# Kernel optimization log

Measured on AMD Instinct MI355X. Metric: run time of the kernel, lower is better.

The kernel has to match this reference:

```python
import jax, jax.numpy as jnp
import numpy as np

IN_DIM = 128
DIM = 32
N_HEADS = 4
LN_EPS = 1e-5


def setup_inputs() -> dict:
    key = jax.random.key(0)
    ks = jax.random.split(key, 10)
    B, N = 1, 256
    z = jax.random.normal(ks[0], (B, N, N, IN_DIM), dtype=jnp.float32)
    src_mask = jax.random.randint(ks[1], (B, N), 0, 2, dtype=jnp.int32)
    s = 1.0 / np.sqrt(IN_DIM)
    # weights stored in (in, out) layout: y = x @ W + b
    return {
        "z": z,
        "src_mask": src_mask,
        "ln_g": jnp.ones((IN_DIM,), jnp.float32),
        "ln_b": jnp.zeros((IN_DIM,), jnp.float32),
        "w_qkv": jax.random.normal(ks[2], (IN_DIM, 3 * N_HEADS * DIM), jnp.float32) * s,
        "w_pair": jax.random.normal(ks[3], (IN_DIM, N_HEADS), jnp.float32) * s,
        "w_gate": jax.random.normal(ks[4], (IN_DIM, IN_DIM), jnp.float32) * s,
        "b_gate": jnp.zeros((IN_DIM,), jnp.float32),
        "w_out": jax.random.normal(ks[5], (N_HEADS * DIM, IN_DIM), jnp.float32) * s,
        "b_out": jnp.zeros((IN_DIM,), jnp.float32),
    }


def reference(z, src_mask, ln_g, ln_b, w_qkv, w_pair, w_gate, b_gate, w_out, b_out):
    B, N, _, _ = z.shape
    H, D = N_HEADS, DIM
    # src_mask: zeros -> -1 (as in the torch in-place assignment)
    m = jnp.where(src_mask == 0, -1.0, 1.0).astype(z.dtype)  # [B, N]
    attn_mask = m[:, :, None] * m[:, None, :]                # [B, N, N], -1 where exactly one is masked
    # LayerNorm over last dim
    mu = jnp.mean(z, axis=-1, keepdims=True)
    var = jnp.mean(jnp.square(z - mu), axis=-1, keepdims=True)
    zn = (z - mu) / jnp.sqrt(var + LN_EPS) * ln_g + ln_b
    # QKV projection (no bias)
    qkv = zn @ w_qkv                                         # [B, N, N, 3*H*D]
    q, k, v = jnp.split(qkv, 3, axis=-1)
    q = q.reshape(B, N, N, H, D)
    k = k.reshape(B, N, N, H, D)
    v = v.reshape(B, N, N, H, D)
    pb = zn @ w_pair                                         # [B, N, N, H] pair bias
    gate = jax.nn.sigmoid(zn @ w_gate + b_gate)              # [B, N, N, IN_DIM]
    scale = float(np.sqrt(D))
    # row-wise triangle attention: attend over j within each row r
    logits = jnp.einsum('brihd,brjhd->brijh', q, k) / scale  # [B, N(r), N(i), N(j), H]
    logits = logits + pb[:, None, :, :, :]                   # bias broadcast over r
    # faithful to torch: masked positions set to -1e-9 (not -inf)
    logits = jnp.where(attn_mask[:, None, :, :, None] == -1, jnp.asarray(-1e-9, logits.dtype), logits)
    attn = jax.nn.softmax(logits, axis=3)
    out = jnp.einsum('brijh,brjhd->brihd', attn, v)          # [B, N, N, H, D]
    out = gate * out.reshape(B, N, N, H * D)
    return out @ w_out + b_out
```

## Files before the change

### kernel.cpp

```cpp
#include <hip/hip_runtime.h>
#include <hip/hip_bf16.h>
#include <math.h>


#define NPOS 65536
#define LN_EPS 1e-5f
#define SCALE_L2E 0.25503487f
#define MASKVAL  -1.4426950e-9f

typedef __attribute__((ext_vector_type(8))) short bf16x8;
typedef __attribute__((ext_vector_type(4))) float f32x4;

__device__ __forceinline__ short f2b(float f) {
    union { float f; unsigned u; } c; c.f = f;
    unsigned r = c.u + 0x7FFFu + ((c.u >> 16) & 1u);
    return (short)(r >> 16);
}
__device__ __forceinline__ unsigned cvt_pk(float lo, float hi) {
    unsigned r;
    asm("v_cvt_pk_bf16_f32 %0, %1, %2" : "=v"(r) : "v"(lo), "v"(hi));
    return r;
}
__device__ __forceinline__ float b2f_lo(unsigned u) {
    union { unsigned u; float f; } c; c.u = u << 16; return c.f;
}
__device__ __forceinline__ float b2f_hi(unsigned u) {
    union { unsigned u; float f; } c; c.u = u & 0xFFFF0000u; return c.f;
}

__global__ void k_prep(const float* __restrict__ wq, const float* __restrict__ wg,
                       const float* __restrict__ wp, const float* __restrict__ wo,
                       const int* __restrict__ smask,
                       short* __restrict__ wT, short* __restrict__ woT,
                       unsigned* __restrict__ mjbg)
{
    const int idx = blockIdx.x * 256 + threadIdx.x;
    const int stride = gridDim.x * 256;
    for (int i = idx; i < 528 * 128; i += stride) {
        const int o = i >> 7, c = i & 127;
        float v;
        if (o < 384)      v = wq[c * 384 + o];
        else if (o < 512) v = wg[c * 128 + (o - 384)];
        else if (o < 516) v = wp[c * 4 + (o - 512)] * 1.4426950408889634f;
        else              v = 0.f;
        wT[i] = f2b(v);
    }
    for (int i = idx; i < 128 * 128; i += stride) {
        const int o = i >> 7, c = i & 127;
        woT[i] = f2b(wo[c * 128 + o]);
    }
    if (blockIdx.x == 0 && threadIdx.x < 8) {
        const int gr = threadIdx.x >> 1, hw = threadIdx.x & 1;
        unsigned wbits = 0;
        for (int b = 0; b < 32; ++b) {
            const int k = hw * 32 + b;
            const int j = (k >> 2) * 16 + gr * 4 + (k & 3);
            if (smask[j] == 0) wbits |= (1u << b);
        }
        mjbg[threadIdx.x] = wbits;
    }
}

__global__ __launch_bounds__(256, 4) void k_proj(
    const float* __restrict__ z, const float* __restrict__ ln_g,
    const float* __restrict__ ln_b, const short* __restrict__ wT,
    const float* __restrict__ b_gate, short* __restrict__ qkbT,
    short* __restrict__ Vtb, float* __restrict__ pbf, short* __restrict__ gate_c)
{
    __shared__ short sBuf[17920];
    const int t = threadIdx.x, w = t >> 6, l = t & 63;
    const int lg = l & 15, gr = l >> 4;
    const int p0 = blockIdx.x * 64;
    const f32x4 zero4 = {0.f, 0.f, 0.f, 0.f};
    short* sV = sBuf;
    short* sZn = sBuf + 9216;
    short* sGt = sZn;

    {
        const int row = t >> 2, q = t & 3;
        const float* zr = z + (size_t)(p0 + row) * 128 + q * 32;
        float v[32];
        float s = 0.f, sq = 0.f;
#pragma unroll
        for (int u = 0; u < 8; ++u) {
            const float4 f = ((const float4*)zr)[u];
            v[u * 4 + 0] = f.x; v[u * 4 + 1] = f.y;
            v[u * 4 + 2] = f.z; v[u * 4 + 3] = f.w;
            s += f.x + f.y + f.z + f.w;
            sq += f.x * f.x + f.y * f.y + f.z * f.z + f.w * f.w;
        }
        s  += __shfl_xor(s, 1, 4);  s  += __shfl_xor(s, 2, 4);
        sq += __shfl_xor(sq, 1, 4); sq += __shfl_xor(sq, 2, 4);
        const float mu = s * (1.f / 128.f);
        const float rstd = rsqrtf(sq * (1.f / 128.f) - mu * mu + LN_EPS);
        short tmp[32];
#pragma unroll
        for (int u = 0; u < 32; ++u) {
            const int c = q * 32 + u;
            tmp[u] = f2b((v[u] - mu) * rstd * ln_g[c] + ln_b[c]);
        }
        uint4* dst = (uint4*)(sZn + row * 136 + q * 32);
#pragma unroll
        for (int u = 0; u < 4; ++u) dst[u] = *(uint4*)&tmp[u * 8];
    }
    __syncthreads();

    bf16x8 a[4][4];
#pragma unroll
    for (int mt = 0; mt < 4; ++mt)
#pragma unroll
        for (int kc = 0; kc < 4; ++kc)
            a[mt][kc] = *(const bf16x8*)(sZn + (mt * 16 + lg) * 136 + kc * 32 + gr * 8);
    __syncthreads();

    short* qblk = qkbT + (size_t)blockIdx.x * 16384;
    for (int nt = w; nt < 16; nt += 4) {
        bf16x8 bfr[4];
#pragma unroll
        for (int kc = 0; kc < 4; ++kc)
            bfr[kc] = *(const bf16x8*)(wT + (size_t)(nt * 16 + lg) * 128 + kc * 32 + gr * 8);
#pragma unroll
        for (int mt = 0; mt < 4; ++mt) {
            f32x4 acc = zero4;
#pragma unroll
            for (int kc = 0; kc < 4; ++kc)
                acc = __builtin_amdgcn_mfma_f32_16x16x32_bf16(bfr[kc], a[mt][kc], acc, 0, 0, 0);
            uint2 pk;
            pk.x = cvt_pk(acc[0], acc[1]);
            pk.y = cvt_pk(acc[2], acc[3]);
            *(uint2*)(qblk + (nt * 4 + mt) * 256 + gr * 64 + lg * 4) = pk;
        }
    }

    for (int nt = 16 + w; nt < 33; nt += 4) {
        bf16x8 bfr[4];
#pragma unroll
        for (int kc = 0; kc < 4; ++kc)
            bfr[kc] = *(const bf16x8*)(wT + (size_t)(nt * 16 + lg) * 128 + kc * 32 + gr * 8);
        const int o = nt * 16 + lg;
#pragma unroll
        for (int mt = 0; mt < 4; ++mt) {
            f32x4 acc = zero4;
#pragma unroll
            for (int kc = 0; kc < 4; ++kc)
                acc = __builtin_amdgcn_mfma_f32_16x16x32_bf16(a[mt][kc], bfr[kc], acc, 0, 0, 0);
            const int pr = p0 + mt * 16 + gr * 4;
            if (o < 384) {
                const int row = o - 256;
                const int jl = mt * 16 + gr * 4;
                const int jp = (jl & 0x23) | ((jl & 12) << 1) | ((jl >> 2) & 4);
                uint2 pk;
                pk.x = cvt_pk(acc[0], acc[1]);
                pk.y = cvt_pk(acc[2], acc[3]);
                *(uint2*)(sV + row * 72 + jp) = pk;
            } else if (o < 512) {
                const int c = o - 384;
                const float bg = b_gate[c];
                uint2 pk;
                pk.x = cvt_pk(1.f / (1.f + __expf(-(acc[0] + bg))),
                              1.f / (1.f + __expf(-(acc[1] + bg))));
                pk.y = cvt_pk(1.f / (1.f + __expf(-(acc[2] + bg))),
                              1.f / (1.f + __expf(-(acc[3] + bg))));
                *(uint2*)(sGt + c * 68 + mt * 16 + gr * 4) = pk;
            } else if (o < 516) {
                *(f32x4*)(pbf + (size_t)(o - 512) * NPOS + pr) = acc;
            }
        }
    }
    __syncthreads();

    {
        const int r = p0 >> 8, jbase = p0 & 255;
        const int row = t >> 1, half = t & 1;
        const short* src = sV + row * 72 + half * 32;
        const int hh = row >> 5, d = row & 31;
        short* dst = Vtb + (((size_t)hh * 256 + r) * 32 + d) * 256 + jbase + half * 32;
#pragma unroll
        for (int u = 0; u < 4; ++u)
            *(uint4*)(dst + u * 8) = *(const uint4*)(src + u * 8);

        const int c = t >> 1;
        const short* gsrc = sGt + c * 68 + half * 32;
        short* gdst = gate_c + (size_t)c * NPOS + p0 + half * 32;
#pragma unroll
        for (int u = 0; u < 8; ++u)
            *(uint2*)(gdst + u * 4) = *(const uint2*)(gsrc + u * 4);
    }
}

__global__ __launch_bounds__(256, 4) void k_attn(
    const short* __restrict__ qkbT, const short* __restrict__ Vtb,
    const float* __restrict__ pbf, const int* __restrict__ smask,
    const short* __restrict__ gate_c, const unsigned* __restrict__ mjbg,
    short* __restrict__ aob)
{
    __shared__ short sK[8192];
    __shared__ short sV[8192];
    const int t = threadIdx.x, wv = t >> 6, l = t & 63;
    const int lg = l & 15, gr = l >> 4;
    const int bid = blockIdx.x;
    const int r = (bid & 7) * 32 + (bid >> 5);
    const int h = (bid >> 3) & 3;
    const int rb = r * 256;
    const f32x4 zero4 = {0.f, 0.f, 0.f, 0.f};
    const unsigned long long mjb = ((const unsigned long long*)mjbg)[gr];
    bf16x8 ones;
#pragma unroll
    for (int u = 0; u < 8; ++u) ones[u] = (short)0x3F80;

#pragma unroll
    for (int it = 0; it < 4; ++it) {
        const int chunk = it * 256 + t;
        const int j = chunk >> 2, dg = chunk & 3;
        const short* kb = qkbT + ((size_t)(r * 4 + (j >> 6))) * 16384
                        + ((8 + h * 2 + (dg >> 1)) * 4 + ((j >> 4) & 3)) * 256
                        + ((dg & 1) * 2) * 64 + (j & 15) * 4;
        uint4 v;
        { const uint2 lo = *(const uint2*)kb, hi = *(const uint2*)(kb + 64);
          v.x = lo.x; v.y = lo.y; v.z = hi.x; v.w = hi.y; }
        *(uint4*)(sK + (((j >> 4) * 4 + dg) * 16 + (j & 15)) * 8) = v;
    }
#pragma unroll
    for (int it = 0; it < 4; ++it) {
        const int d = it * 8 + (t >> 5), kcgr = t & 31;
        const uint4 v = *(const uint4*)(Vtb + (((size_t)h * 256 + r) * 32 + d) * 256 + kcgr * 8);
        *(uint4*)(sV + (kcgr * 32 + (d ^ (kcgr & 7))) * 8) = v;
    }
    __syncthreads();

    for (int tl = 0; tl < 4; ++tl) {
        const int i0 = wv * 64 + tl * 16;
        bf16x8 qf;
        {
            const short* qb = qkbT + ((size_t)(r * 4 + wv)) * 16384
                            + ((h * 2 + (gr >> 1)) * 4 + tl) * 256
                            + ((gr & 1) * 2) * 64 + lg * 4;
            union { bf16x8 v; uint2 u2[2]; } qu;
            qu.u2[0] = *(const uint2*)qb;
            qu.u2[1] = *(const uint2*)(qb + 64);
            qf = qu.v;
        }
        const uint2 gu0 = *(const uint2*)(gate_c + (size_t)(h * 32 + lg) * NPOS + rb + i0 + gr * 4);
        const uint2 gu1 = *(const uint2*)(gate_c + (size_t)(h * 32 + 16 + lg) * NPOS + rb + i0 + gr * 4);
        const bool bi = smask[i0 + lg] == 0;
        const unsigned long long mjc = bi ? ~mjb : mjb;
        const unsigned mwA = (unsigned)mjc;
        const unsigned mwB = (unsigned)(mjc >> 32);
        const float* pbrow = pbf + (size_t)h * NPOS + (size_t)(i0 + lg) * 256;

        f32x4 o0 = zero4, o1 = zero4, o2 = zero4;

        unsigned pkA[16];
#pragma unroll
        for (int nt = 0; nt < 8; ++nt) {
            const bf16x8 kf = *(const bf16x8*)(sK + ((nt * 4 + gr) * 16 + lg) * 8);
            const f32x4 pbv = *(const f32x4*)(pbrow + nt * 16 + gr * 4);
            const f32x4 s4 = __builtin_amdgcn_mfma_f32_16x16x32_bf16(kf, qf, zero4, 0, 0, 0);
            float pv[4];
#pragma unroll
            for (int reg = 0; reg < 4; ++reg) {
                float lv = fmaf(s4[reg], SCALE_L2E, pbv[reg]);
                lv = ((mwA >> (nt * 4 + reg)) & 1) ? MASKVAL : lv;
                pv[reg] = exp2f(lv);
            }
            pkA[nt * 2 + 0] = cvt_pk(pv[0], pv[1]);
            pkA[nt * 2 + 1] = cvt_pk(pv[2], pv[3]);
        }
        __builtin_amdgcn_s_setprio(1);
#pragma unroll
        for (int kc = 0; kc < 4; ++kc) {
            const int kcgr = kc * 4 + gr, c7 = kcgr & 7;
            const bf16x8 pa = *(const bf16x8*)(&pkA[kc * 4]);
            const bf16x8 v0 = *(const bf16x8*)(sV + (kcgr * 32 + (lg ^ c7)) * 8);
            const bf16x8 v1 = *(const bf16x8*)(sV + (kcgr * 32 + 16 + (lg ^ c7)) * 8);
            o0 = __builtin_amdgcn_mfma_f32_16x16x32_bf16(pa, v0, o0, 0, 0, 0);
            o1 = __builtin_amdgcn_mfma_f32_16x16x32_bf16(pa, v1, o1, 0, 0, 0);
            o2 = __builtin_amdgcn_mfma_f32_16x16x32_bf16(pa, ones, o2, 0, 0, 0);
        }
        __builtin_amdgcn_s_setprio(0);

        unsigned pkB[16];
#pragma unroll
        for (int nt = 8; nt < 16; ++nt) {
            const bf16x8 kf = *(const bf16x8*)(sK + ((nt * 4 + gr) * 16 + lg) * 8);
            const f32x4 pbv = *(const f32x4*)(pbrow + nt * 16 + gr * 4);
            const f32x4 s4 = __builtin_amdgcn_mfma_f32_16x16x32_bf16(kf, qf, zero4, 0, 0, 0);
            float pv[4];
#pragma unroll
            for (int reg = 0; reg < 4; ++reg) {
                float lv = fmaf(s4[reg], SCALE_L2E, pbv[reg]);
                lv = ((mwB >> ((nt - 8) * 4 + reg)) & 1) ? MASKVAL : lv;
                pv[reg] = exp2f(lv);
            }
            pkB[(nt - 8) * 2 + 0] = cvt_pk(pv[0], pv[1]);
            pkB[(nt - 8) * 2 + 1] = cvt_pk(pv[2], pv[3]);
        }
        __builtin_amdgcn_s_setprio(1);
#pragma unroll
        for (int kc = 4; kc < 8; ++kc) {
            const int kcgr = kc * 4 + gr, c7 = kcgr & 7;
            const bf16x8 pa = *(const bf16x8*)(&pkB[(kc - 4) * 4]);
            const bf16x8 v0 = *(const bf16x8*)(sV + (kcgr * 32 + (lg ^ c7)) * 8);
            const bf16x8 v1 = *(const bf16x8*)(sV + (kcgr * 32 + 16 + (lg ^ c7)) * 8);
            o0 = __builtin_amdgcn_mfma_f32_16x16x32_bf16(pa, v0, o0, 0, 0, 0);
            o1 = __builtin_amdgcn_mfma_f32_16x16x32_bf16(pa, v1, o1, 0, 0, 0);
            o2 = __builtin_amdgcn_mfma_f32_16x16x32_bf16(pa, ones, o2, 0, 0, 0);
        }
        __builtin_amdgcn_s_setprio(0);

#pragma unroll
        for (int reg = 0; reg < 4; ++reg) {
            const int p = rb + i0 + gr * 4 + reg;
            const unsigned w0 = (reg < 2) ? gu0.x : gu0.y;
            const unsigned w1 = (reg < 2) ? gu1.x : gu1.y;
            const float g0 = (reg & 1) ? b2f_hi(w0) : b2f_lo(w0);
            const float g1 = (reg & 1) ? b2f_hi(w1) : b2f_lo(w1);
            const float inv = 1.f / o2[reg];
            short* dst = aob + ((size_t)h * NPOS + p) * 32;
            dst[lg]      = f2b(o0[reg] * inv * g0);
            dst[16 + lg] = f2b(o1[reg] * inv * g1);
        }
    }
}

__global__ __launch_bounds__(256) void k_out(
    const short* __restrict__ aob, const short* __restrict__ woT,
    const float* __restrict__ b_out, float* __restrict__ out)
{
    const int t = threadIdx.x, w = t >> 6, l = t & 63;
    const int lg = l & 15, gr = l >> 4;
    const int bid = blockIdx.x;
    const int r = (bid & 7) * 32 + (bid >> 5);
    const int qtr = (bid >> 3) & 3;
    const int p0 = r * 256 + qtr * 64;
    const f32x4 zero4 = {0.f, 0.f, 0.f, 0.f};

    bf16x8 a[4][4];
#pragma unroll
    for (int mt = 0; mt < 4; ++mt)
#pragma unroll
        for (int kc = 0; kc < 4; ++kc)
            a[mt][kc] = *(const bf16x8*)(aob + ((size_t)kc * NPOS + p0 + mt * 16 + lg) * 32 + gr * 8);

    for (int nt = w; nt < 8; nt += 4) {
        bf16x8 bw[4];
#pragma unroll
        for (int kc = 0; kc < 4; ++kc)
            bw[kc] = *(const bf16x8*)(woT + (size_t)(nt * 16 + lg) * 128 + kc * 32 + gr * 8);
        const int o = nt * 16 + lg;
        const float bo = b_out[o];
#pragma unroll
        for (int mt = 0; mt < 4; ++mt) {
            f32x4 c = zero4;
#pragma unroll
            for (int kc = 0; kc < 4; ++kc)
                c = __builtin_amdgcn_mfma_f32_16x16x32_bf16(a[mt][kc], bw[kc], c, 0, 0, 0);
#pragma unroll
            for (int reg = 0; reg < 4; ++reg)
                out[(size_t)(p0 + mt * 16 + gr * 4 + reg) * 128 + o] = c[reg] + bo;
        }
    }
}

extern "C" void kernel_launch(void* const* d_in, const int* in_sizes, int n_in,
                              void* d_out, int out_size, void* d_ws, size_t ws_size,
                              hipStream_t stream)
{
    const float* z      = (const float*)d_in[0];
    const int*   smask  = (const int*)d_in[1];
    const float* ln_g   = (const float*)d_in[2];
    const float* ln_b   = (const float*)d_in[3];
    const float* w_qkv  = (const float*)d_in[4];
    const float* w_pair = (const float*)d_in[5];
    const float* w_gate = (const float*)d_in[6];
    const float* b_gate = (const float*)d_in[7];
    const float* w_out  = (const float*)d_in[8];
    const float* b_out  = (const float*)d_in[9];
    float* out = (float*)d_out;

    short* ws      = (short*)d_ws;
    short* qkbT    = ws;
    short* Vtb     = qkbT + (size_t)NPOS * 256;
    short* wT      = Vtb + (size_t)8388608;
    short* woT     = wT + 528 * 128;
    unsigned* mjbg = (unsigned*)(woT + 128 * 128);
    float* pbf     = (float*)(mjbg + 16);
    short* gate_c  = (short*)(pbf + (size_t)4 * NPOS);
    short* aob     = gate_c + (size_t)128 * NPOS;

    k_prep<<<64, 256, 0, stream>>>(w_qkv, w_gate, w_pair, w_out, smask, wT, woT, mjbg);
    k_proj<<<NPOS / 64, 256, 0, stream>>>(z, ln_g, ln_b, wT, b_gate, qkbT, Vtb, pbf, gate_c);
    k_attn<<<1024, 256, 0, stream>>>(qkbT, Vtb, pbf, smask, gate_c, mjbg, aob);
    k_out<<<NPOS / 64, 256, 0, stream>>>(aob, woT, b_out, out);
}
```

Before: 105.3 us.

## Store gate and pair bias in fragment-tiled bf16 layouts for attention loads

```diff
diff --git a/kernel.cpp b/kernel.cpp
--- a/kernel.cpp
+++ b/kernel.cpp
@@ -65,7 +65,7 @@
     const float* __restrict__ z, const float* __restrict__ ln_g,
     const float* __restrict__ ln_b, const short* __restrict__ wT,
     const float* __restrict__ b_gate, short* __restrict__ qkbT,
-    short* __restrict__ Vtb, float* __restrict__ pbf, short* __restrict__ gate_c)
+    short* __restrict__ Vtb, short* __restrict__ pbT, short* __restrict__ gT)
 {
     __shared__ short sBuf[17920];
     const int t = threadIdx.x, w = t >> 6, l = t & 63;
@@ -74,7 +74,6 @@
     const f32x4 zero4 = {0.f, 0.f, 0.f, 0.f};
     short* sV = sBuf;
     short* sZn = sBuf + 9216;
-    short* sGt = sZn;
 
     {
         const int row = t >> 2, q = t & 3;
@@ -132,6 +131,8 @@
         }
     }
 
+    const int rI   = p0 >> 8;
+    const int jbas = p0 & 255;
     for (int nt = 16 + w; nt < 33; nt += 4) {
         bf16x8 bfr[4];
 #pragma unroll
@@ -144,7 +145,6 @@
 #pragma unroll
             for (int kc = 0; kc < 4; ++kc)
                 acc = __builtin_amdgcn_mfma_f32_16x16x32_bf16(a[mt][kc], bfr[kc], acc, 0, 0, 0);
-            const int pr = p0 + mt * 16 + gr * 4;
             if (o < 384) {
                 const int row = o - 256;
                 const int jl = mt * 16 + gr * 4;
@@ -156,42 +156,46 @@
             } else if (o < 512) {
                 const int c = o - 384;
                 const float bg = b_gate[c];
+                const int hh = (nt - 24) >> 1, cp = (nt - 24) & 1;
+                const int it = (jbas >> 4) + mt;
                 uint2 pk;
                 pk.x = cvt_pk(1.f / (1.f + __expf(-(acc[0] + bg))),
                               1.f / (1.f + __expf(-(acc[1] + bg))));
                 pk.y = cvt_pk(1.f / (1.f + __expf(-(acc[2] + bg))),
                               1.f / (1.f + __expf(-(acc[3] + bg))));
-                *(uint2*)(sGt + c * 68 + mt * 16 + gr * 4) = pk;
+                *(uint2*)(gT + ((((size_t)rI * 4 + hh) * 2 + cp) * 16 + it) * 256
+                             + (lg * 4 + gr) * 4) = pk;
             } else if (o < 516) {
-                *(f32x4*)(pbf + (size_t)(o - 512) * NPOS + pr) = acc;
+                if (lg < 4) {
+                    const int itI = rI >> 4, ipI = rI & 15;
+                    const int j0 = jbas + mt * 16 + gr * 4;
+                    const int ntj = j0 >> 4, grj = (j0 >> 2) & 3;
+                    uint2 pk;
+                    pk.x = cvt_pk(acc[0], acc[1]);
+                    pk.y = cvt_pk(acc[2], acc[3]);
+                    *(uint2*)(pbT + (((size_t)(lg * 16 + itI) * 16) + ntj) * 256
+                                 + (ipI * 4 + grj) * 4) = pk;
+                }
             }
         }
     }
     __syncthreads();
 
     {
-        const int r = p0 >> 8, jbase = p0 & 255;
         const int row = t >> 1, half = t & 1;
         const short* src = sV + row * 72 + half * 32;
         const int hh = row >> 5, d = row & 31;
-        short* dst = Vtb + (((size_t)hh * 256 + r) * 32 + d) * 256 + jbase + half * 32;
+        short* dst = Vtb + (((size_t)hh * 256 + rI) * 32 + d) * 256 + jbas + half * 32;
 #pragma unroll
         for (int u = 0; u < 4; ++u)
             *(uint4*)(dst + u * 8) = *(const uint4*)(src + u * 8);
-
-        const int c = t >> 1;
-        const short* gsrc = sGt + c * 68 + half * 32;
-        short* gdst = gate_c + (size_t)c * NPOS + p0 + half * 32;
-#pragma unroll
-        for (int u = 0; u < 8; ++u)
-            *(uint2*)(gdst + u * 4) = *(const uint2*)(gsrc + u * 4);
     }
 }
 
 __global__ __launch_bounds__(256, 4) void k_attn(
     const short* __restrict__ qkbT, const short* __restrict__ Vtb,
-    const float* __restrict__ pbf, const int* __restrict__ smask,
-    const short* __restrict__ gate_c, const unsigned* __restrict__ mjbg,
+    const short* __restrict__ pbT, const int* __restrict__ smask,
+    const short* __restrict__ gT, const unsigned* __restrict__ mjbg,
     short* __restrict__ aob)
 {
     __shared__ short sK[8192];
@@ -228,8 +232,11 @@
     }
     __syncthreads();
 
+    const int lanelin = (lg * 4 + gr) * 4;
+
     for (int tl = 0; tl < 4; ++tl) {
         const int i0 = wv * 64 + tl * 16;
+        const int it = wv * 4 + tl;
         bf16x8 qf;
         {
             const short* qb = qkbT + ((size_t)(r * 4 + wv)) * 16384
@@ -240,13 +247,12 @@
             qu.u2[1] = *(const uint2*)(qb + 64);
             qf = qu.v;
         }
-        const uint2 gu0 = *(const uint2*)(gate_c + (size_t)(h * 32 + lg) * NPOS + rb + i0 + gr * 4);
-        const uint2 gu1 = *(const uint2*)(gate_c + (size_t)(h * 32 + 16 + lg) * NPOS + rb + i0 + gr * 4);
+        const short* gbase = gT + ((((size_t)r * 4 + h) * 2) * 16 + it) * 256 + lanelin;
+        const uint2 gu0 = *(const uint2*)gbase;
+        const uint2 gu1 = *(const uint2*)(gbase + 4096);
         const bool bi = smask[i0 + lg] == 0;
         const unsigned long long mjc = bi ? ~mjb : mjb;
-        const unsigned mwA = (unsigned)mjc;
-        const unsigned mwB = (unsigned)(mjc >> 32);
-        const float* pbrow = pbf + (size_t)h * NPOS + (size_t)(i0 + lg) * 256;
+        const short* pbase = pbT + (((size_t)(h * 16 + it)) * 16) * 256 + lanelin;
 
         f32x4 o0 = zero4, o1 = zero4, o2 = zero4;
 
@@ -254,13 +260,14 @@
 #pragma unroll
         for (int nt = 0; nt < 8; ++nt) {
             const bf16x8 kf = *(const bf16x8*)(sK + ((nt * 4 + gr) * 16 + lg) * 8);
-            const f32x4 pbv = *(const f32x4*)(pbrow + nt * 16 + gr * 4);
+            const uint2 pbp = *(const uint2*)(pbase + nt * 256);
             const f32x4 s4 = __builtin_amdgcn_mfma_f32_16x16x32_bf16(kf, qf, zero4, 0, 0, 0);
+            const float pbv[4] = { b2f_lo(pbp.x), b2f_hi(pbp.x), b2f_lo(pbp.y), b2f_hi(pbp.y) };
             float pv[4];
 #pragma unroll
             for (int reg = 0; reg < 4; ++reg) {
                 float lv = fmaf(s4[reg], SCALE_L2E, pbv[reg]);
-                lv = ((mwA >> (nt * 4 + reg)) & 1) ? MASKVAL : lv;
+                lv = ((mjc >> (nt * 4 + reg)) & 1) ? MASKVAL : lv;
                 pv[reg] = exp2f(lv);
             }
             pkA[nt * 2 + 0] = cvt_pk(pv[0], pv[1]);
@@ -283,13 +290,14 @@
 #pragma unroll
         for (int nt = 8; nt < 16; ++nt) {
             const bf16x8 kf = *(const bf16x8*)(sK + ((nt * 4 + gr) * 16 + lg) * 8);
-            const f32x4 pbv = *(const f32x4*)(pbrow + nt * 16 + gr * 4);
+            const uint2 pbp = *(const uint2*)(pbase + nt * 256);
             const f32x4 s4 = __builtin_amdgcn_mfma_f32_16x16x32_bf16(kf, qf, zero4, 0, 0, 0);
+            const float pbv[4] = { b2f_lo(pbp.x), b2f_hi(pbp.x), b2f_lo(pbp.y), b2f_hi(pbp.y) };
             float pv[4];
 #pragma unroll
             for (int reg = 0; reg < 4; ++reg) {
                 float lv = fmaf(s4[reg], SCALE_L2E, pbv[reg]);
-                lv = ((mwB >> ((nt - 8) * 4 + reg)) & 1) ? MASKVAL : lv;
+                lv = ((mjc >> (nt * 4 + reg)) & 1) ? MASKVAL : lv;
                 pv[reg] = exp2f(lv);
             }
             pkB[(nt - 8) * 2 + 0] = cvt_pk(pv[0], pv[1]);
@@ -384,12 +392,12 @@
     short* wT      = Vtb + (size_t)8388608;
     short* woT     = wT + 528 * 128;
     unsigned* mjbg = (unsigned*)(woT + 128 * 128);
-    float* pbf     = (float*)(mjbg + 16);
-    short* gate_c  = (short*)(pbf + (size_t)4 * NPOS);
-    short* aob     = gate_c + (size_t)128 * NPOS;
+    short* pbT     = (short*)(mjbg + 16);
+    short* gT      = pbT + 262144;
+    short* aob     = gT + (size_t)8388608;
 
     k_prep<<<64, 256, 0, stream>>>(w_qkv, w_gate, w_pair, w_out, smask, wT, woT, mjbg);
-    k_proj<<<NPOS / 64, 256, 0, stream>>>(z, ln_g, ln_b, wT, b_gate, qkbT, Vtb, pbf, gate_c);
-    k_attn<<<1024, 256, 0, stream>>>(qkbT, Vtb, pbf, smask, gate_c, mjbg, aob);
+    k_proj<<<NPOS / 64, 256, 0, stream>>>(z, ln_g, ln_b, wT, b_gate, qkbT, Vtb, pbT, gT);
+    k_attn<<<1024, 256, 0, stream>>>(qkbT, Vtb, pbT, smask, gT, mjbg, aob);
     k_out<<<NPOS / 64, 256, 0, stream>>>(aob, woT, b_out, out);
 }
```

Result: faster. 94.66 us (-10.1%).
